# Optimization experiments

Measured on AMD Instinct MI355X. Metric: run time of the kernel, lower is better.

The kernel has to match this reference:

```python
import jax, jax.numpy as jnp
import numpy as np
import math

D_MODEL = 1024
N_HEADS = 16
HEAD_DIM = D_MODEL // N_HEADS
N_LEVELS = 4
B = 8
MAX_LEN = 1024
LN_EPS = 1e-5


def setup_inputs() -> dict:
    key = jax.random.key(0)
    ks = jax.random.split(key, 6)
    lengths = np.array([1024, 768, 512, 896, 640, 1024, 576, 704], dtype=np.int32)
    N = int(lengths.sum())  # 6144
    batch_offsets = jnp.asarray(np.concatenate([[0], np.cumsum(lengths)]).astype(np.int32))
    x = jax.random.normal(ks[0], (N, D_MODEL), jnp.float32)
    levels = jax.random.randint(ks[1], (N, 1), 0, N_LEVELS).astype(jnp.float32)
    coords = jax.random.uniform(ks[2], (N, 2), jnp.float32) * 64.0
    positions = jnp.concatenate([levels, coords], axis=-1)  # [N, 3] = (level, y, x)
    ln_gamma = jnp.ones((D_MODEL,), jnp.float32)
    ln_beta = jnp.zeros((D_MODEL,), jnp.float32)
    w_qkv = jax.random.normal(ks[3], (D_MODEL, 3 * D_MODEL), jnp.float32) / math.sqrt(D_MODEL)
    w_out = jax.random.normal(ks[4], (D_MODEL, D_MODEL), jnp.float32) / math.sqrt(D_MODEL)
    # learned per-level, per-head rotary frequencies for 2 spatial coords
    base = 10.0 ** (-2.0 * np.arange(HEAD_DIM // 2) / HEAD_DIM)  # rope_theta = 10.0
    rope_freqs = (jnp.asarray(base, jnp.float32)[None, None, :, None]
                  * (1.0 + 0.1 * jax.random.normal(ks[5], (N_LEVELS, N_HEADS, HEAD_DIM // 2, 2), jnp.float32)))
    return {"x": x, "positions": positions, "batch_offsets": batch_offsets,
            "ln_gamma": ln_gamma, "ln_beta": ln_beta, "w_qkv": w_qkv,
            "w_out": w_out, "rope_freqs": rope_freqs}


def _layernorm(x, g, b):
    mu = jnp.mean(x, axis=-1, keepdims=True)
    var = jnp.mean(jnp.square(x - mu), axis=-1, keepdims=True)
    return (x - mu) * jax.lax.rsqrt(var + LN_EPS) * g + b


def _forward(x, positions, batch_offsets, ln_gamma, ln_beta, w_qkv, w_out, rope_freqs):
    N = x.shape[0]
    residual = x
    h = _layernorm(x, ln_gamma, ln_beta)
    q, k, v = jnp.split(h @ w_qkv, 3, axis=-1)  # each [N, D]

    # ragged -> padded batch layout
    tok = jnp.arange(N)
    batch_ids = jnp.searchsorted(batch_offsets[1:], tok, side='right')  # [N]
    pos_in_seq = tok - batch_offsets[batch_ids]                         # [N]
    lengths = batch_offsets[1:] - batch_offsets[:-1]                    # [B]
    valid = jnp.arange(MAX_LEN)[None, :] < lengths[:, None]             # [B, L]

    def pad(t, fill=0.0):
        out = jnp.full((B, MAX_LEN) + t.shape[1:], fill, t.dtype)
        return out.at[batch_ids, pos_in_seq].set(t)

    qp = pad(q).reshape(B, MAX_LEN, N_HEADS, HEAD_DIM)
    kp = pad(k).reshape(B, MAX_LEN, N_HEADS, HEAD_DIM)
    vp = pad(v).reshape(B, MAX_LEN, N_HEADS, HEAD_DIM)
    posp = pad(positions, fill=1.0)  # padded positions filled with ones (as in torch code)

    # multilevel RoPE: per-level learned freqs over 2 spatial coords
    lvl = jnp.clip(posp[..., 0].astype(jnp.int32), 0, N_LEVELS - 1)  # [B, L]
    f = rope_freqs[lvl]                                              # [B, L, H, K, 2]
    ang = jnp.einsum('blhkc,blc->blhk', f, posp[..., 1:])            # [B, L, H, K]
    cos, sin = jnp.cos(ang), jnp.sin(ang)

    def rot(t):  # rotate consecutive pairs of head_dim
        t = t.reshape(B, MAX_LEN, N_HEADS, HEAD_DIM // 2, 2)
        a, b = t[..., 0], t[..., 1]
        return jnp.stack([a * cos - b * sin, a * sin + b * cos], axis=-1).reshape(
            B, MAX_LEN, N_HEADS, HEAD_DIM)

    qr, kr = rot(qp), rot(kp)

    # masked SDPA (padded keys excluded; padded query rows are dropped on un-pad)
    scale = 1.0 / math.sqrt(HEAD_DIM)
    scores = jnp.einsum('blhd,bmhd->bhlm', qr, kr) * scale
    scores = jnp.where(valid[:, None, None, :], scores, jnp.float32(-1e9))
    attn = jax.nn.softmax(scores, axis=-1)
    o = jnp.einsum('bhlm,bmhd->blhd', attn, vp).reshape(B, MAX_LEN, D_MODEL)

    o = o[batch_ids, pos_in_seq]  # back to packed [N, D]
    return o @ w_out + residual


def reference(x, positions, batch_offsets, ln_gamma, ln_beta, w_qkv, w_out, rope_freqs):
    return _forward(x, positions, batch_offsets, ln_gamma, ln_beta, w_qkv, w_out, rope_freqs)
```

## Files before the change

### kernel.cpp

```cpp
#include <hip/hip_runtime.h>


typedef float  f32x4  __attribute__((ext_vector_type(4)));
typedef __bf16 bf16x8 __attribute__((ext_vector_type(8)));
typedef __bf16 bf16x4 __attribute__((ext_vector_type(4)));
typedef short  s16x4  __attribute__((ext_vector_type(4)));
typedef short  s16x8  __attribute__((ext_vector_type(8)));
typedef unsigned short u16x4 __attribute__((ext_vector_type(4)));

typedef __attribute__((address_space(1))) void as1_void_t;
typedef __attribute__((address_space(3))) void as3_void_t;

static __device__ __forceinline__ unsigned short f2bf(float f) {
  unsigned int u = __float_as_uint(f);
  u += 0x7fffu + ((u >> 16) & 1u);
  return (unsigned short)(u >> 16);
}
static __device__ __forceinline__ float bf2f(unsigned short s) {
  return __uint_as_float(((unsigned int)s) << 16);
}

static __device__ __forceinline__ void gload_lds16(const void* g, void* l) {
  __builtin_amdgcn_global_load_lds((as1_void_t*)g, (as3_void_t*)l, 16, 0, 0);
}

static __device__ __forceinline__ f32x4 mfma32(bf16x8 a, bf16x8 b, f32x4 c) {
  return __builtin_amdgcn_mfma_f32_16x16x32_bf16(a, b, c, 0, 0, 0);
}
static __device__ __forceinline__ f32x4 mfma16(s16x4 a, s16x4 b, f32x4 c) {
  return __builtin_amdgcn_mfma_f32_16x16x16bf16_1k(a, b, c, 0, 0, 0);
}

__global__ __launch_bounds__(256) void ln_kernel(
    const float* __restrict__ x, const float* __restrict__ gamma,
    const float* __restrict__ beta, unsigned short* __restrict__ h, int Ntok) {
  int row  = blockIdx.x * 4 + (threadIdx.x >> 6);
  int lane = threadIdx.x & 63;
  const float* xr = x + (size_t)row * 1024;
  f32x4 v[4];
  float s = 0.f, ss = 0.f;
#pragma unroll
  for (int c = 0; c < 4; ++c) {
    v[c] = *(const f32x4*)(xr + c * 256 + lane * 4);
#pragma unroll
    for (int j = 0; j < 4; ++j) { s += v[c][j]; ss += v[c][j] * v[c][j]; }
  }
#pragma unroll
  for (int d = 1; d < 64; d <<= 1) {
    s  += __shfl_xor(s, d);
    ss += __shfl_xor(ss, d);
  }
  float mu  = s * (1.f / 1024.f);
  float var = ss * (1.f / 1024.f) - mu * mu;
  float inv = rsqrtf(var + 1e-5f);
#pragma unroll
  for (int c = 0; c < 4; ++c) {
    f32x4 gv = *(const f32x4*)(gamma + c * 256 + lane * 4);
    f32x4 bv = *(const f32x4*)(beta  + c * 256 + lane * 4);
    u16x4 hv;
#pragma unroll
    for (int j = 0; j < 4; ++j) hv[j] = f2bf((v[c][j] - mu) * inv * gv[j] + bv[j]);
    *(u16x4*)(h + (size_t)row * 1024 + c * 256 + lane * 4) = hv;
  }
}

__global__ __launch_bounds__(256) void transpose_bf16(
    const float* __restrict__ in, unsigned short* __restrict__ out, int R, int C) {
  __shared__ unsigned short tile[64][65];
  int c0 = blockIdx.x * 64, r0 = blockIdx.y * 64;
  int t = threadIdx.x;
  int tr = t >> 6, tc = t & 63;
#pragma unroll
  for (int i = 0; i < 16; ++i) {
    int rr = i * 4 + tr;
    tile[tc][rr] = f2bf(in[(size_t)(r0 + rr) * C + c0 + tc]);
  }
  __syncthreads();
#pragma unroll
  for (int i = 0; i < 16; ++i) {
    int cc = i * 4 + tr;
    out[(size_t)(c0 + cc) * R + r0 + tc] = tile[cc][tc];
  }
}

template <int MODE>
__global__ __launch_bounds__(256) void gemm_bt(
    const unsigned short* __restrict__ A, const unsigned short* __restrict__ Bt,
    const float* __restrict__ residual, float* __restrict__ Cf,
    unsigned short* __restrict__ Cqkv, int M, int Ncols, int K) {
  __shared__ unsigned short Alds[128 * 32];
  __shared__ unsigned short Blds[128 * 32];
  int n0 = blockIdx.x * 128, m0 = blockIdx.y * 128;
  int t = threadIdx.x, lane = t & 63, wave = t >> 6;
  int wr = wave >> 1, wc = wave & 1;
  int r = lane & 15, g = lane >> 4;
  f32x4 acc[4][4] = {};

  int srow = lane >> 2;
  int scol = (lane & 3) * 8;

  for (int k0 = 0; k0 < K; k0 += 32) {
    __syncthreads();
#pragma unroll
    for (int c = 0; c < 2; ++c) {
      int seg = wave * 2 + c;
      gload_lds16(A  + (size_t)(m0 + seg * 16 + srow) * K + k0 + scol,
                  Alds + seg * 16 * 32);
      gload_lds16(Bt + (size_t)(n0 + seg * 16 + srow) * K + k0 + scol,
                  Blds + seg * 16 * 32);
    }
    __syncthreads();
    bf16x8 a[4], b[4];
#pragma unroll
    for (int m = 0; m < 4; ++m)
      a[m] = *(const bf16x8*)(Alds + (wr * 64 + m * 16 + r) * 32 + g * 8);
#pragma unroll
    for (int n = 0; n < 4; ++n)
      b[n] = *(const bf16x8*)(Blds + (wc * 64 + n * 16 + r) * 32 + g * 8);
#pragma unroll
    for (int m = 0; m < 4; ++m)
#pragma unroll
      for (int n = 0; n < 4; ++n)
        acc[m][n] = mfma32(a[m], b[n], acc[m][n]);
  }

#pragma unroll
  for (int mi = 0; mi < 4; ++mi) {
    int grow0 = m0 + wr * 64 + mi * 16 + g * 4;
#pragma unroll
    for (int ni = 0; ni < 4; ++ni) {
      int gcol = n0 + wc * 64 + ni * 16 + r;
      f32x4 v = acc[mi][ni];
#pragma unroll
      for (int e = 0; e < 4; ++e) {
        int grow = grow0 + e;
        if (MODE == 0) {
          Cf[(size_t)grow * Ncols + gcol] =
              v[e] + residual[(size_t)grow * Ncols + gcol];
        } else {
          int which = gcol >> 10, rem = gcol & 1023, hh = rem >> 6, d = rem & 63;
          Cqkv[((size_t)(which * 16 + hh) * M + grow) * 64 + d] = f2bf(v[e]);
        }
      }
    }
  }
}

__global__ __launch_bounds__(256) void rope_kernel(
    unsigned short* __restrict__ QKV, const float* __restrict__ pos,
    const float* __restrict__ freqs, int Ntok) {
  int t = blockIdx.x * 256 + threadIdx.x;
  if (t >= Ntok * 512) return;
  int kk = t & 31, h = (t >> 5) & 15, i = t >> 9;
  float lvlf = pos[i * 3 + 0];
  float py   = pos[i * 3 + 1];
  float px   = pos[i * 3 + 2];
  int lvl = (int)lvlf;
  lvl = lvl < 0 ? 0 : (lvl > 3 ? 3 : lvl);
  const float* fp = freqs + (((lvl * 16 + h) * 32 + kk) << 1);
  float ang = fp[0] * py + fp[1] * px;
  float s, c;
  __sincosf(ang, &s, &c);
  size_t qoff = ((size_t)h * Ntok + i) * 64 + 2 * kk;
  size_t koff = qoff + (size_t)16 * Ntok * 64;
  unsigned int q2 = *(const unsigned int*)(QKV + qoff);
  float qa = bf2f((unsigned short)(q2 & 0xffff));
  float qb = bf2f((unsigned short)(q2 >> 16));
  *(unsigned int*)(QKV + qoff) =
      (unsigned int)f2bf(qa * c - qb * s) | ((unsigned int)f2bf(qa * s + qb * c) << 16);
  unsigned int k2 = *(const unsigned int*)(QKV + koff);
  float ka = bf2f((unsigned short)(k2 & 0xffff));
  float kb = bf2f((unsigned short)(k2 >> 16));
  *(unsigned int*)(QKV + koff) =
      (unsigned int)f2bf(ka * c - kb * s) | ((unsigned int)f2bf(ka * s + kb * c) << 16);
}

__global__ __launch_bounds__(128, 3) void attn_kernel(
    const unsigned short* __restrict__ QKV, const int* __restrict__ boff,
    unsigned short* __restrict__ O, int Ntok) {
  __shared__ unsigned short Klds[64][72];
  __shared__ unsigned short Vt[64][72];
  const float SCALE_LOG2 = 0.125f * 1.44269504088896340736f;

  int bid = blockIdx.x;
  int x = bid & 7, i = bid >> 3;
  int qblk = i & 15;
  int p = x + 8 * (i >> 4);
  int h = p & 15, b = p >> 4;
  int off = boff[b], len = boff[b + 1] - off;
  int q0 = qblk * 64;
  if (q0 >= len) return;
  int t = threadIdx.x, lane = t & 63, wave = t >> 6;
  int r = lane & 15, g = lane >> 4;
  const unsigned short* Qg = QKV + (size_t)h * Ntok * 64;
  const unsigned short* Kg = QKV + (size_t)(16 + h) * Ntok * 64;
  const unsigned short* Vg = QKV + (size_t)(32 + h) * Ntok * 64;
  int qmax = off + len - 1;

  bf16x8 qf[2][2];
#pragma unroll
  for (int qi = 0; qi < 2; ++qi) {
    int qtok = off + q0 + wave * 32 + qi * 16 + r;
    if (qtok > qmax) qtok = qmax;
#pragma unroll
    for (int c = 0; c < 2; ++c)
      qf[qi][c] = *(const bf16x8*)(Qg + (size_t)qtok * 64 + c * 32 + g * 8);
  }

  float m[2] = {-1e30f, -1e30f}, lsum[2] = {0.f, 0.f};
  f32x4 o[2][4] = {};

  int krow = t >> 1, kseg = t & 1;
  int vp = t & 31, vdc = t >> 5;

  s16x8 kr[4], va0, va1, vb0, vb1;
  {
    int ktok = off + krow; if (ktok > qmax) ktok = qmax;
#pragma unroll
    for (int c = 0; c < 4; ++c)
      kr[c] = *(const s16x8*)(Kg + (size_t)ktok * 64 + kseg * 32 + c * 8);
    int va = off + 2 * vp, vb = va + 1;
    if (va > qmax) va = qmax;
    if (vb > qmax) vb = qmax;
    va0 = *(const s16x8*)(Vg + (size_t)va * 64 + vdc * 16);
    va1 = *(const s16x8*)(Vg + (size_t)va * 64 + vdc * 16 + 8);
    vb0 = *(const s16x8*)(Vg + (size_t)vb * 64 + vdc * 16);
    vb1 = *(const s16x8*)(Vg + (size_t)vb * 64 + vdc * 16 + 8);
  }

  for (int kt = 0; kt < len; kt += 64) {
    __syncthreads();
#pragma unroll
    for (int c = 0; c < 4; ++c)
      *(s16x8*)&Klds[krow][kseg * 32 + c * 8] = kr[c];
#pragma unroll
    for (int j = 0; j < 8; ++j) {
      unsigned int p0 = (unsigned int)(unsigned short)va0[j] |
                        ((unsigned int)(unsigned short)vb0[j] << 16);
      unsigned int p1 = (unsigned int)(unsigned short)va1[j] |
                        ((unsigned int)(unsigned short)vb1[j] << 16);
      *(unsigned int*)&Vt[vdc * 16 + j][2 * vp]     = p0;
      *(unsigned int*)&Vt[vdc * 16 + 8 + j][2 * vp] = p1;
    }
    int ktn = kt + 64;
    if (ktn < len) {
      int ktok = off + ktn + krow; if (ktok > qmax) ktok = qmax;
#pragma unroll
      for (int c = 0; c < 4; ++c)
        kr[c] = *(const s16x8*)(Kg + (size_t)ktok * 64 + kseg * 32 + c * 8);
      int va = off + ktn + 2 * vp, vb = va + 1;
      if (va > qmax) va = qmax;
      if (vb > qmax) vb = qmax;
      va0 = *(const s16x8*)(Vg + (size_t)va * 64 + vdc * 16);
      va1 = *(const s16x8*)(Vg + (size_t)va * 64 + vdc * 16 + 8);
      vb0 = *(const s16x8*)(Vg + (size_t)vb * 64 + vdc * 16);
      vb1 = *(const s16x8*)(Vg + (size_t)vb * 64 + vdc * 16 + 8);
    }
    __syncthreads();

    f32x4 s[2][4];
    __builtin_amdgcn_s_setprio(1);
#pragma unroll
    for (int sub = 0; sub < 4; ++sub) {
      bf16x8 ka0 = *(const bf16x8*)(&Klds[sub * 16 + r][g * 8]);
      bf16x8 ka1 = *(const bf16x8*)(&Klds[sub * 16 + r][32 + g * 8]);
#pragma unroll
      for (int qi = 0; qi < 2; ++qi) {
        f32x4 acc = {};
        acc = mfma32(ka0, qf[qi][0], acc);
        acc = mfma32(ka1, qf[qi][1], acc);
        s[qi][sub] = acc;
      }
    }
    __builtin_amdgcn_s_setprio(0);

    bool tail = (kt + 64 > len);
    s16x4 pf[2][4];
#pragma unroll
    for (int qi = 0; qi < 2; ++qi) {
      float sc[4][4];
      float tmax = -1e30f;
#pragma unroll
      for (int sub = 0; sub < 4; ++sub)
#pragma unroll
        for (int e = 0; e < 4; ++e) {
          float v = s[qi][sub][e];
          if (tail && (kt + sub * 16 + 4 * g + e >= len)) v = -1e30f;
          sc[sub][e] = v;
          tmax = fmaxf(tmax, v);
        }
      float mq = m[qi];
      if (!__all(tmax * SCALE_LOG2 <= mq + 8.f)) {
        float tm = tmax * SCALE_LOG2;
        tm = fmaxf(tm, __shfl_xor(tm, 16));
        tm = fmaxf(tm, __shfl_xor(tm, 32));
        float mnew = fmaxf(mq, tm);
        float alpha = exp2f(mq - mnew);
        lsum[qi] *= alpha;
        m[qi] = mnew; mq = mnew;
        float al[4];
#pragma unroll
        for (int e = 0; e < 4; ++e) al[e] = __shfl(alpha, 4 * g + e);
#pragma unroll
        for (int dt = 0; dt < 4; ++dt)
#pragma unroll
          for (int e = 0; e < 4; ++e) o[qi][dt][e] *= al[e];
      }
      float psum = 0.f;
#pragma unroll
      for (int sub = 0; sub < 4; ++sub) {
        float pv[4];
        bf16x4 pb;
#pragma unroll
        for (int e = 0; e < 4; ++e) {
          pv[e] = exp2f(fmaf(sc[sub][e], SCALE_LOG2, -mq));
          psum += pv[e];
          pb[e] = (__bf16)pv[e];
        }
        pf[qi][sub] = __builtin_bit_cast(s16x4, pb);
      }
      psum += __shfl_xor(psum, 16);
      psum += __shfl_xor(psum, 32);
      lsum[qi] += psum;
    }

    __builtin_amdgcn_s_setprio(1);
#pragma unroll
    for (int dt = 0; dt < 4; ++dt)
#pragma unroll
      for (int sub = 0; sub < 4; ++sub) {
        s16x4 vf = *(const s16x4*)(&Vt[dt * 16 + r][sub * 16 + 4 * g]);
#pragma unroll
        for (int qi = 0; qi < 2; ++qi)
          o[qi][dt] = mfma16(pf[qi][sub], vf, o[qi][dt]);
      }
    __builtin_amdgcn_s_setprio(0);
  }

#pragma unroll
  for (int qi = 0; qi < 2; ++qi) {
    float inv = 1.0f / lsum[qi];
    float il[4];
#pragma unroll
    for (int e = 0; e < 4; ++e) il[e] = __shfl(inv, 4 * g + e);
#pragma unroll
    for (int dt = 0; dt < 4; ++dt)
#pragma unroll
      for (int e = 0; e < 4; ++e) {
        int tl = q0 + wave * 32 + qi * 16 + 4 * g + e;
        if (tl < len)
          O[(size_t)(off + tl) * 1024 + h * 64 + dt * 16 + r] =
              f2bf(o[qi][dt][e] * il[e]);
      }
  }
}

extern "C" void kernel_launch(void* const* d_in, const int* in_sizes, int n_in,
                              void* d_out, int out_size, void* d_ws, size_t ws_size,
                              hipStream_t stream) {
  const float* x     = (const float*)d_in[0];
  const float* pos   = (const float*)d_in[1];
  const int*   boff  = (const int*)d_in[2];
  const float* gamma = (const float*)d_in[3];
  const float* beta  = (const float*)d_in[4];
  const float* wqkv  = (const float*)d_in[5];
  const float* wout  = (const float*)d_in[6];
  const float* freqs = (const float*)d_in[7];
  float* out = (float*)d_out;
  int N  = in_sizes[0] / 1024;
  int Bn = in_sizes[2] - 1;

  char* ws = (char*)d_ws;
  unsigned short* wqkvT = (unsigned short*)ws;
  unsigned short* woutT = (unsigned short*)(ws + (size_t)3072 * 1024 * 2);
  unsigned short* QKV   = (unsigned short*)(ws + (size_t)3072 * 1024 * 2 +
                                            (size_t)1024 * 1024 * 2);
  size_t qkvBytes = (size_t)48 * N * 64 * 2;
  unsigned short* hbuf = (unsigned short*)((char*)QKV + qkvBytes);
  unsigned short* Obuf = hbuf;

  ln_kernel<<<N / 4, 256, 0, stream>>>(x, gamma, beta, hbuf, N);
  transpose_bf16<<<dim3(3072 / 64, 1024 / 64), 256, 0, stream>>>(wqkv, wqkvT, 1024, 3072);
  transpose_bf16<<<dim3(1024 / 64, 1024 / 64), 256, 0, stream>>>(wout, woutT, 1024, 1024);
  gemm_bt<1><<<dim3(3072 / 128, N / 128), 256, 0, stream>>>(
      hbuf, wqkvT, nullptr, nullptr, QKV, N, 3072, 1024);
  rope_kernel<<<(N * 512) / 256, 256, 0, stream>>>(QKV, pos, freqs, N);
  attn_kernel<<<Bn * 16 * 16, 128, 0, stream>>>(QKV, boff, Obuf, N);
  gemm_bt<0><<<dim3(1024 / 128, N / 128), 256, 0, stream>>>(
      Obuf, woutT, x, out, nullptr, N, 1024, 1024);
}
```

Before: 189.5 us.

## Fuse RoPE into QKV GEMM epilogue, store V transposed, compute softmax sums via MFMA

Rotary embedding moves into the QKV GEMM epilogue, using a lane shuffle to fetch each pair partner, so the separate rope kernel and its read-modify-write pass over Q and K go away. V is written transposed (head-dim major, token minor) so the attention kernel can copy it straight into LDS without the per-element pair packing. The softmax row sum is now an MFMA of P against a ones vector instead of shuffle reductions. Risks: the transposed V loads clamp reads near the sequence tail, and bf16-rounded P now feeds the denominator as well as the numerator.

```diff
diff --git a/kernel.cpp b/kernel.cpp
--- a/kernel.cpp
+++ b/kernel.cpp
@@ -87,7 +87,8 @@
 __global__ __launch_bounds__(256) void gemm_bt(
     const unsigned short* __restrict__ A, const unsigned short* __restrict__ Bt,
     const float* __restrict__ residual, float* __restrict__ Cf,
-    unsigned short* __restrict__ Cqkv, int M, int Ncols, int K) {
+    unsigned short* __restrict__ Cqkv, const float* __restrict__ pos,
+    const float* __restrict__ freqs, int M, int Ncols, int K) {
   __shared__ unsigned short Alds[128 * 32];
   __shared__ unsigned short Blds[128 * 32];
   int n0 = blockIdx.x * 128, m0 = blockIdx.y * 128;
@@ -124,55 +125,73 @@
         acc[m][n] = mfma32(a[m], b[n], acc[m][n]);
   }
 
-#pragma unroll
-  for (int mi = 0; mi < 4; ++mi) {
-    int grow0 = m0 + wr * 64 + mi * 16 + g * 4;
-#pragma unroll
-    for (int ni = 0; ni < 4; ++ni) {
-      int gcol = n0 + wc * 64 + ni * 16 + r;
-      f32x4 v = acc[mi][ni];
-#pragma unroll
-      for (int e = 0; e < 4; ++e) {
-        int grow = grow0 + e;
-        if (MODE == 0) {
-          Cf[(size_t)grow * Ncols + gcol] =
-              v[e] + residual[(size_t)grow * Ncols + gcol];
-        } else {
-          int which = gcol >> 10, rem = gcol & 1023, hh = rem >> 6, d = rem & 63;
-          Cqkv[((size_t)(which * 16 + hh) * M + grow) * 64 + d] = f2bf(v[e]);
+  if (MODE == 0) {
+#pragma unroll
+    for (int mi = 0; mi < 4; ++mi) {
+      int grow0 = m0 + wr * 64 + mi * 16 + g * 4;
+#pragma unroll
+      for (int ni = 0; ni < 4; ++ni) {
+        int gcol = n0 + wc * 64 + ni * 16 + r;
+        f32x4 v = acc[mi][ni];
+#pragma unroll
+        for (int e = 0; e < 4; ++e)
+          Cf[(size_t)(grow0 + e) * Ncols + gcol] =
+              v[e] + residual[(size_t)(grow0 + e) * Ncols + gcol];
+      }
+    }
+  } else {
+    int which = n0 >> 10;
+    if (which == 2) {
+      unsigned short* VtG = Cqkv + (size_t)32 * M * 64;
+#pragma unroll
+      for (int mi = 0; mi < 4; ++mi) {
+        int grow0 = m0 + wr * 64 + mi * 16 + g * 4;
+#pragma unroll
+        for (int ni = 0; ni < 4; ++ni) {
+          int gcol = n0 + wc * 64 + ni * 16 + r;
+          int rem = gcol & 1023, hh = rem >> 6, d = rem & 63;
+          f32x4 v = acc[mi][ni];
+          u16x4 hv;
+#pragma unroll
+          for (int e = 0; e < 4; ++e) hv[e] = f2bf(v[e]);
+          *(u16x4*)(VtG + (size_t)(hh * 64 + d) * M + grow0) = hv;
         }
       }
-    }
-  }
-}
-
-__global__ __launch_bounds__(256) void rope_kernel(
-    unsigned short* __restrict__ QKV, const float* __restrict__ pos,
-    const float* __restrict__ freqs, int Ntok) {
-  int t = blockIdx.x * 256 + threadIdx.x;
-  if (t >= Ntok * 512) return;
-  int kk = t & 31, h = (t >> 5) & 15, i = t >> 9;
-  float lvlf = pos[i * 3 + 0];
-  float py   = pos[i * 3 + 1];
-  float px   = pos[i * 3 + 2];
-  int lvl = (int)lvlf;
-  lvl = lvl < 0 ? 0 : (lvl > 3 ? 3 : lvl);
-  const float* fp = freqs + (((lvl * 16 + h) * 32 + kk) << 1);
-  float ang = fp[0] * py + fp[1] * px;
-  float s, c;
-  __sincosf(ang, &s, &c);
-  size_t qoff = ((size_t)h * Ntok + i) * 64 + 2 * kk;
-  size_t koff = qoff + (size_t)16 * Ntok * 64;
-  unsigned int q2 = *(const unsigned int*)(QKV + qoff);
-  float qa = bf2f((unsigned short)(q2 & 0xffff));
-  float qb = bf2f((unsigned short)(q2 >> 16));
-  *(unsigned int*)(QKV + qoff) =
-      (unsigned int)f2bf(qa * c - qb * s) | ((unsigned int)f2bf(qa * s + qb * c) << 16);
-  unsigned int k2 = *(const unsigned int*)(QKV + koff);
-  float ka = bf2f((unsigned short)(k2 & 0xffff));
-  float kb = bf2f((unsigned short)(k2 >> 16));
-  *(unsigned int*)(QKV + koff) =
-      (unsigned int)f2bf(ka * c - kb * s) | ((unsigned int)f2bf(ka * s + kb * c) << 16);
+    } else {
+#pragma unroll
+      for (int mi = 0; mi < 4; ++mi) {
+        int grow0 = m0 + wr * 64 + mi * 16 + g * 4;
+        float py[4], px[4];
+        int lv[4];
+#pragma unroll
+        for (int e = 0; e < 4; ++e) {
+          int tk = grow0 + e;
+          int l = (int)pos[tk * 3 + 0];
+          lv[e] = l < 0 ? 0 : (l > 3 ? 3 : l);
+          py[e] = pos[tk * 3 + 1];
+          px[e] = pos[tk * 3 + 2];
+        }
+#pragma unroll
+        for (int ni = 0; ni < 4; ++ni) {
+          int gcol = n0 + wc * 64 + ni * 16 + r;
+          int rem = gcol & 1023, hh = rem >> 6, d = rem & 63;
+          int kk = d >> 1, par = d & 1;
+          f32x4 v = acc[mi][ni];
+#pragma unroll
+          for (int e = 0; e < 4; ++e) {
+            float other = __shfl_xor(v[e], 1);
+            const float* fp = freqs + (((lv[e] * 16 + hh) * 32 + kk) << 1);
+            float ang = fp[0] * py[e] + fp[1] * px[e];
+            float sn, cs;
+            __sincosf(ang, &sn, &cs);
+            float vc = v[e] * cs;
+            float res = par ? fmaf(other, sn, vc) : fmaf(other, -sn, vc);
+            Cqkv[((size_t)(which * 16 + hh) * M + grow0 + e) * 64 + d] = f2bf(res);
+          }
+        }
+      }
+    }
+  }
 }
 
 __global__ __launch_bounds__(128, 3) void attn_kernel(
@@ -181,6 +200,7 @@
   __shared__ unsigned short Klds[64][72];
   __shared__ unsigned short Vt[64][72];
   const float SCALE_LOG2 = 0.125f * 1.44269504088896340736f;
+  const s16x4 ones16 = {(short)0x3F80, (short)0x3F80, (short)0x3F80, (short)0x3F80};
 
   int bid = blockIdx.x;
   int x = bid & 7, i = bid >> 3;
@@ -194,7 +214,7 @@
   int r = lane & 15, g = lane >> 4;
   const unsigned short* Qg = QKV + (size_t)h * Ntok * 64;
   const unsigned short* Kg = QKV + (size_t)(16 + h) * Ntok * 64;
-  const unsigned short* Vg = QKV + (size_t)(32 + h) * Ntok * 64;
+  const unsigned short* VtG = QKV + (size_t)32 * Ntok * 64;
   int qmax = off + len - 1;
 
   bf16x8 qf[2][2];
@@ -207,54 +227,46 @@
       qf[qi][c] = *(const bf16x8*)(Qg + (size_t)qtok * 64 + c * 32 + g * 8);
   }
 
-  float m[2] = {-1e30f, -1e30f}, lsum[2] = {0.f, 0.f};
+  float m[2] = {-1e30f, -1e30f};
   f32x4 o[2][4] = {};
-
-  int krow = t >> 1, kseg = t & 1;
-  int vp = t & 31, vdc = t >> 5;
-
-  s16x8 kr[4], va0, va1, vb0, vb1;
+  f32x4 o_sum[2] = {};
+
+  int srow = t >> 1, sseg = t & 1;
+  const unsigned short* Vrow = VtG + (size_t)(h * 64 + srow) * Ntok;
+
+  s16x8 kr[4], vr[4];
   {
-    int ktok = off + krow; if (ktok > qmax) ktok = qmax;
+    int ktok = off + srow; if (ktok > qmax) ktok = qmax;
 #pragma unroll
     for (int c = 0; c < 4; ++c)
-      kr[c] = *(const s16x8*)(Kg + (size_t)ktok * 64 + kseg * 32 + c * 8);
-    int va = off + 2 * vp, vb = va + 1;
-    if (va > qmax) va = qmax;
-    if (vb > qmax) vb = qmax;
-    va0 = *(const s16x8*)(Vg + (size_t)va * 64 + vdc * 16);
-    va1 = *(const s16x8*)(Vg + (size_t)va * 64 + vdc * 16 + 8);
-    vb0 = *(const s16x8*)(Vg + (size_t)vb * 64 + vdc * 16);
-    vb1 = *(const s16x8*)(Vg + (size_t)vb * 64 + vdc * 16 + 8);
+      kr[c] = *(const s16x8*)(Kg + (size_t)ktok * 64 + sseg * 32 + c * 8);
+    int ts = sseg * 32;
+    if (ts + 8 > len) ts = len - 8;
+#pragma unroll
+    for (int c = 0; c < 4; ++c) {
+      int tc = ts + c * 8; if (tc + 8 > len) tc = len - 8;
+      vr[c] = *(const s16x8*)(Vrow + off + tc);
+    }
   }
 
   for (int kt = 0; kt < len; kt += 64) {
     __syncthreads();
 #pragma unroll
-    for (int c = 0; c < 4; ++c)
-      *(s16x8*)&Klds[krow][kseg * 32 + c * 8] = kr[c];
-#pragma unroll
-    for (int j = 0; j < 8; ++j) {
-      unsigned int p0 = (unsigned int)(unsigned short)va0[j] |
-                        ((unsigned int)(unsigned short)vb0[j] << 16);
-      unsigned int p1 = (unsigned int)(unsigned short)va1[j] |
-                        ((unsigned int)(unsigned short)vb1[j] << 16);
-      *(unsigned int*)&Vt[vdc * 16 + j][2 * vp]     = p0;
-      *(unsigned int*)&Vt[vdc * 16 + 8 + j][2 * vp] = p1;
+    for (int c = 0; c < 4; ++c) {
+      *(s16x8*)&Klds[srow][sseg * 32 + c * 8] = kr[c];
+      *(s16x8*)&Vt[srow][sseg * 32 + c * 8]   = vr[c];
     }
     int ktn = kt + 64;
     if (ktn < len) {
-      int ktok = off + ktn + krow; if (ktok > qmax) ktok = qmax;
+      int ktok = off + ktn + srow; if (ktok > qmax) ktok = qmax;
 #pragma unroll
       for (int c = 0; c < 4; ++c)
-        kr[c] = *(const s16x8*)(Kg + (size_t)ktok * 64 + kseg * 32 + c * 8);
-      int va = off + ktn + 2 * vp, vb = va + 1;
-      if (va > qmax) va = qmax;
-      if (vb > qmax) vb = qmax;
-      va0 = *(const s16x8*)(Vg + (size_t)va * 64 + vdc * 16);
-      va1 = *(const s16x8*)(Vg + (size_t)va * 64 + vdc * 16 + 8);
-      vb0 = *(const s16x8*)(Vg + (size_t)vb * 64 + vdc * 16);
-      vb1 = *(const s16x8*)(Vg + (size_t)vb * 64 + vdc * 16 + 8);
+        kr[c] = *(const s16x8*)(Kg + (size_t)ktok * 64 + sseg * 32 + c * 8);
+#pragma unroll
+      for (int c = 0; c < 4; ++c) {
+        int tc = ktn + sseg * 32 + c * 8; if (tc + 8 > len) tc = len - 8;
+        vr[c] = *(const s16x8*)(Vrow + off + tc);
+      }
     }
     __syncthreads();
 
@@ -279,16 +291,19 @@
 #pragma unroll
     for (int qi = 0; qi < 2; ++qi) {
       float sc[4][4];
-      float tmax = -1e30f;
-#pragma unroll
-      for (int sub = 0; sub < 4; ++sub)
+      float ms[4];
+#pragma unroll
+      for (int sub = 0; sub < 4; ++sub) {
 #pragma unroll
         for (int e = 0; e < 4; ++e) {
           float v = s[qi][sub][e];
           if (tail && (kt + sub * 16 + 4 * g + e >= len)) v = -1e30f;
           sc[sub][e] = v;
-          tmax = fmaxf(tmax, v);
         }
+        ms[sub] = fmaxf(fmaxf(sc[sub][0], sc[sub][1]),
+                        fmaxf(sc[sub][2], sc[sub][3]));
+      }
+      float tmax = fmaxf(fmaxf(ms[0], ms[1]), fmaxf(ms[2], ms[3]));
       float mq = m[qi];
       if (!__all(tmax * SCALE_LOG2 <= mq + 8.f)) {
         float tm = tmax * SCALE_LOG2;
@@ -296,35 +311,30 @@
         tm = fmaxf(tm, __shfl_xor(tm, 32));
         float mnew = fmaxf(mq, tm);
         float alpha = exp2f(mq - mnew);
-        lsum[qi] *= alpha;
         m[qi] = mnew; mq = mnew;
-        float al[4];
-#pragma unroll
-        for (int e = 0; e < 4; ++e) al[e] = __shfl(alpha, 4 * g + e);
+#pragma unroll
+        for (int e = 0; e < 4; ++e) o_sum[qi][e] *= alpha;
 #pragma unroll
         for (int dt = 0; dt < 4; ++dt)
 #pragma unroll
-          for (int e = 0; e < 4; ++e) o[qi][dt][e] *= al[e];
-      }
-      float psum = 0.f;
+          for (int e = 0; e < 4; ++e) o[qi][dt][e] *= alpha;
+      }
 #pragma unroll
       for (int sub = 0; sub < 4; ++sub) {
-        float pv[4];
         bf16x4 pb;
 #pragma unroll
-        for (int e = 0; e < 4; ++e) {
-          pv[e] = exp2f(fmaf(sc[sub][e], SCALE_LOG2, -mq));
-          psum += pv[e];
-          pb[e] = (__bf16)pv[e];
-        }
+        for (int e = 0; e < 4; ++e)
+          pb[e] = (__bf16)exp2f(fmaf(sc[sub][e], SCALE_LOG2, -mq));
         pf[qi][sub] = __builtin_bit_cast(s16x4, pb);
       }
-      psum += __shfl_xor(psum, 16);
-      psum += __shfl_xor(psum, 32);
-      lsum[qi] += psum;
     }
 
     __builtin_amdgcn_s_setprio(1);
+#pragma unroll
+    for (int sub = 0; sub < 4; ++sub) {
+      o_sum[0] = mfma16(pf[0][sub], ones16, o_sum[0]);
+      o_sum[1] = mfma16(pf[1][sub], ones16, o_sum[1]);
+    }
 #pragma unroll
     for (int dt = 0; dt < 4; ++dt)
 #pragma unroll
@@ -339,10 +349,9 @@
 
 #pragma unroll
   for (int qi = 0; qi < 2; ++qi) {
-    float inv = 1.0f / lsum[qi];
     float il[4];
 #pragma unroll
-    for (int e = 0; e < 4; ++e) il[e] = __shfl(inv, 4 * g + e);
+    for (int e = 0; e < 4; ++e) il[e] = 1.0f / o_sum[qi][e];
 #pragma unroll
     for (int dt = 0; dt < 4; ++dt)
 #pragma unroll
@@ -383,9 +392,8 @@
   transpose_bf16<<<dim3(3072 / 64, 1024 / 64), 256, 0, stream>>>(wqkv, wqkvT, 1024, 3072);
   transpose_bf16<<<dim3(1024 / 64, 1024 / 64), 256, 0, stream>>>(wout, woutT, 1024, 1024);
   gemm_bt<1><<<dim3(3072 / 128, N / 128), 256, 0, stream>>>(
-      hbuf, wqkvT, nullptr, nullptr, QKV, N, 3072, 1024);
-  rope_kernel<<<(N * 512) / 256, 256, 0, stream>>>(QKV, pos, freqs, N);
+      hbuf, wqkvT, nullptr, nullptr, QKV, pos, freqs, N, 3072, 1024);
   attn_kernel<<<Bn * 16 * 16, 128, 0, stream>>>(QKV, boff, Obuf, N);
   gemm_bt<0><<<dim3(1024 / 128, N / 128), 256, 0, stream>>>(
-      Obuf, woutT, x, out, nullptr, N, 1024, 1024);
-}
+      Obuf, woutT, x, out, nullptr, nullptr, nullptr, N, 1024, 1024);
+}
```

After: 200.1 us. 5.6% more time.

## Pre-transpose V in a separate kernel and compute softmax row sums via MFMA

Applied to the files above, without the earlier changes.

A new kernel transposes V into a head-major, dimension-by-token global buffer. The attention kernel can then stage V tiles into LDS with plain vector copies instead of interleaving token pairs per element. The softmax denominator is now accumulated by an MFMA against a vector of bf16 ones, which drops the per-tile shuffle reductions and the alpha broadcast shuffles. This costs an extra launch plus a full read and write of V, and the output buffer now reuses the original V region.

```diff
diff --git a/kernel.cpp b/kernel.cpp
--- a/kernel.cpp
+++ b/kernel.cpp
@@ -175,12 +175,42 @@
       (unsigned int)f2bf(ka * c - kb * s) | ((unsigned int)f2bf(ka * s + kb * c) << 16);
 }
 
+__global__ __launch_bounds__(256) void vtrans_kernel(
+    const unsigned short* __restrict__ Vp, unsigned short* __restrict__ VtG,
+    int Ntok) {
+  __shared__ unsigned short tile[64][72];
+  int blk = blockIdx.x;
+  int h = blk & 15, t0 = (blk >> 4) * 64;
+  int t = threadIdx.x;
+  {
+    int tok = t >> 2, dc = (t & 3) * 16;
+    const unsigned short* src = Vp + ((size_t)h * Ntok + t0 + tok) * 64 + dc;
+    *(s16x8*)&tile[tok][dc]     = *(const s16x8*)src;
+    *(s16x8*)&tile[tok][dc + 8] = *(const s16x8*)(src + 8);
+  }
+  __syncthreads();
+  {
+    int d = t >> 2, tc = (t & 3) * 16;
+    s16x8 o0, o1;
+#pragma unroll
+    for (int j = 0; j < 8; ++j) {
+      o0[j] = (short)tile[tc + j][d];
+      o1[j] = (short)tile[tc + 8 + j][d];
+    }
+    unsigned short* dst = VtG + (size_t)(h * 64 + d) * Ntok + t0 + tc;
+    *(s16x8*)dst       = o0;
+    *(s16x8*)(dst + 8) = o1;
+  }
+}
+
 __global__ __launch_bounds__(128, 3) void attn_kernel(
-    const unsigned short* __restrict__ QKV, const int* __restrict__ boff,
+    const unsigned short* __restrict__ QKV,
+    const unsigned short* __restrict__ VtG, const int* __restrict__ boff,
     unsigned short* __restrict__ O, int Ntok) {
   __shared__ unsigned short Klds[64][72];
   __shared__ unsigned short Vt[64][72];
   const float SCALE_LOG2 = 0.125f * 1.44269504088896340736f;
+  const s16x4 ones16 = {(short)0x3F80, (short)0x3F80, (short)0x3F80, (short)0x3F80};
 
   int bid = blockIdx.x;
   int x = bid & 7, i = bid >> 3;
@@ -194,7 +224,6 @@
   int r = lane & 15, g = lane >> 4;
   const unsigned short* Qg = QKV + (size_t)h * Ntok * 64;
   const unsigned short* Kg = QKV + (size_t)(16 + h) * Ntok * 64;
-  const unsigned short* Vg = QKV + (size_t)(32 + h) * Ntok * 64;
   int qmax = off + len - 1;
 
   bf16x8 qf[2][2];
@@ -207,54 +236,44 @@
       qf[qi][c] = *(const bf16x8*)(Qg + (size_t)qtok * 64 + c * 32 + g * 8);
   }
 
-  float m[2] = {-1e30f, -1e30f}, lsum[2] = {0.f, 0.f};
+  float m[2] = {-1e30f, -1e30f};
   f32x4 o[2][4] = {};
-
-  int krow = t >> 1, kseg = t & 1;
-  int vp = t & 31, vdc = t >> 5;
-
-  s16x8 kr[4], va0, va1, vb0, vb1;
+  f32x4 o_sum[2] = {};
+
+  int srow = t >> 1, sseg = t & 1;
+  const unsigned short* Vrow = VtG + (size_t)(h * 64 + srow) * Ntok;
+
+  s16x8 kr[4], vr[4];
   {
-    int ktok = off + krow; if (ktok > qmax) ktok = qmax;
+    int ktok = off + srow; if (ktok > qmax) ktok = qmax;
 #pragma unroll
     for (int c = 0; c < 4; ++c)
-      kr[c] = *(const s16x8*)(Kg + (size_t)ktok * 64 + kseg * 32 + c * 8);
-    int va = off + 2 * vp, vb = va + 1;
-    if (va > qmax) va = qmax;
-    if (vb > qmax) vb = qmax;
-    va0 = *(const s16x8*)(Vg + (size_t)va * 64 + vdc * 16);
-    va1 = *(const s16x8*)(Vg + (size_t)va * 64 + vdc * 16 + 8);
-    vb0 = *(const s16x8*)(Vg + (size_t)vb * 64 + vdc * 16);
-    vb1 = *(const s16x8*)(Vg + (size_t)vb * 64 + vdc * 16 + 8);
+      kr[c] = *(const s16x8*)(Kg + (size_t)ktok * 64 + sseg * 32 + c * 8);
+#pragma unroll
+    for (int c = 0; c < 4; ++c) {
+      int tc = sseg * 32 + c * 8; if (tc + 8 > len) tc = len - 8;
+      vr[c] = *(const s16x8*)(Vrow + off + tc);
+    }
   }
 
   for (int kt = 0; kt < len; kt += 64) {
     __syncthreads();
 #pragma unroll
-    for (int c = 0; c < 4; ++c)
-      *(s16x8*)&Klds[krow][kseg * 32 + c * 8] = kr[c];
-#pragma unroll
-    for (int j = 0; j < 8; ++j) {
-      unsigned int p0 = (unsigned int)(unsigned short)va0[j] |
-                        ((unsigned int)(unsigned short)vb0[j] << 16);
-      unsigned int p1 = (unsigned int)(unsigned short)va1[j] |
-                        ((unsigned int)(unsigned short)vb1[j] << 16);
-      *(unsigned int*)&Vt[vdc * 16 + j][2 * vp]     = p0;
-      *(unsigned int*)&Vt[vdc * 16 + 8 + j][2 * vp] = p1;
+    for (int c = 0; c < 4; ++c) {
+      *(s16x8*)&Klds[srow][sseg * 32 + c * 8] = kr[c];
+      *(s16x8*)&Vt[srow][sseg * 32 + c * 8]   = vr[c];
     }
     int ktn = kt + 64;
     if (ktn < len) {
-      int ktok = off + ktn + krow; if (ktok > qmax) ktok = qmax;
+      int ktok = off + ktn + srow; if (ktok > qmax) ktok = qmax;
 #pragma unroll
       for (int c = 0; c < 4; ++c)
-        kr[c] = *(const s16x8*)(Kg + (size_t)ktok * 64 + kseg * 32 + c * 8);
-      int va = off + ktn + 2 * vp, vb = va + 1;
-      if (va > qmax) va = qmax;
-      if (vb > qmax) vb = qmax;
-      va0 = *(const s16x8*)(Vg + (size_t)va * 64 + vdc * 16);
-      va1 = *(const s16x8*)(Vg + (size_t)va * 64 + vdc * 16 + 8);
-      vb0 = *(const s16x8*)(Vg + (size_t)vb * 64 + vdc * 16);
-      vb1 = *(const s16x8*)(Vg + (size_t)vb * 64 + vdc * 16 + 8);
+        kr[c] = *(const s16x8*)(Kg + (size_t)ktok * 64 + sseg * 32 + c * 8);
+#pragma unroll
+      for (int c = 0; c < 4; ++c) {
+        int tc = ktn + sseg * 32 + c * 8; if (tc + 8 > len) tc = len - 8;
+        vr[c] = *(const s16x8*)(Vrow + off + tc);
+      }
     }
     __syncthreads();
 
@@ -279,16 +298,19 @@
 #pragma unroll
     for (int qi = 0; qi < 2; ++qi) {
       float sc[4][4];
-      float tmax = -1e30f;
-#pragma unroll
-      for (int sub = 0; sub < 4; ++sub)
+      float ms[4];
+#pragma unroll
+      for (int sub = 0; sub < 4; ++sub) {
 #pragma unroll
         for (int e = 0; e < 4; ++e) {
           float v = s[qi][sub][e];
           if (tail && (kt + sub * 16 + 4 * g + e >= len)) v = -1e30f;
           sc[sub][e] = v;
-          tmax = fmaxf(tmax, v);
         }
+        ms[sub] = fmaxf(fmaxf(sc[sub][0], sc[sub][1]),
+                        fmaxf(sc[sub][2], sc[sub][3]));
+      }
+      float tmax = fmaxf(fmaxf(ms[0], ms[1]), fmaxf(ms[2], ms[3]));
       float mq = m[qi];
       if (!__all(tmax * SCALE_LOG2 <= mq + 8.f)) {
         float tm = tmax * SCALE_LOG2;
@@ -296,35 +318,30 @@
         tm = fmaxf(tm, __shfl_xor(tm, 32));
         float mnew = fmaxf(mq, tm);
         float alpha = exp2f(mq - mnew);
-        lsum[qi] *= alpha;
         m[qi] = mnew; mq = mnew;
-        float al[4];
-#pragma unroll
-        for (int e = 0; e < 4; ++e) al[e] = __shfl(alpha, 4 * g + e);
+#pragma unroll
+        for (int e = 0; e < 4; ++e) o_sum[qi][e] *= alpha;
 #pragma unroll
         for (int dt = 0; dt < 4; ++dt)
 #pragma unroll
-          for (int e = 0; e < 4; ++e) o[qi][dt][e] *= al[e];
-      }
-      float psum = 0.f;
+          for (int e = 0; e < 4; ++e) o[qi][dt][e] *= alpha;
+      }
 #pragma unroll
       for (int sub = 0; sub < 4; ++sub) {
-        float pv[4];
         bf16x4 pb;
 #pragma unroll
-        for (int e = 0; e < 4; ++e) {
-          pv[e] = exp2f(fmaf(sc[sub][e], SCALE_LOG2, -mq));
-          psum += pv[e];
-          pb[e] = (__bf16)pv[e];
-        }
+        for (int e = 0; e < 4; ++e)
+          pb[e] = (__bf16)exp2f(fmaf(sc[sub][e], SCALE_LOG2, -mq));
         pf[qi][sub] = __builtin_bit_cast(s16x4, pb);
       }
-      psum += __shfl_xor(psum, 16);
-      psum += __shfl_xor(psum, 32);
-      lsum[qi] += psum;
     }
 
     __builtin_amdgcn_s_setprio(1);
+#pragma unroll
+    for (int sub = 0; sub < 4; ++sub) {
+      o_sum[0] = mfma16(pf[0][sub], ones16, o_sum[0]);
+      o_sum[1] = mfma16(pf[1][sub], ones16, o_sum[1]);
+    }
 #pragma unroll
     for (int dt = 0; dt < 4; ++dt)
 #pragma unroll
@@ -339,10 +356,9 @@
 
 #pragma unroll
   for (int qi = 0; qi < 2; ++qi) {
-    float inv = 1.0f / lsum[qi];
     float il[4];
 #pragma unroll
-    for (int e = 0; e < 4; ++e) il[e] = __shfl(inv, 4 * g + e);
+    for (int e = 0; e < 4; ++e) il[e] = 1.0f / o_sum[qi][e];
 #pragma unroll
     for (int dt = 0; dt < 4; ++dt)
 #pragma unroll
@@ -377,7 +393,9 @@
                                             (size_t)1024 * 1024 * 2);
   size_t qkvBytes = (size_t)48 * N * 64 * 2;
   unsigned short* hbuf = (unsigned short*)((char*)QKV + qkvBytes);
-  unsigned short* Obuf = hbuf;
+  unsigned short* VtG  = hbuf;
+  unsigned short* Vp   = QKV + (size_t)32 * N * 64;
+  unsigned short* Obuf = Vp;
 
   ln_kernel<<<N / 4, 256, 0, stream>>>(x, gamma, beta, hbuf, N);
   transpose_bf16<<<dim3(3072 / 64, 1024 / 64), 256, 0, stream>>>(wqkv, wqkvT, 1024, 3072);
@@ -385,7 +403,8 @@
   gemm_bt<1><<<dim3(3072 / 128, N / 128), 256, 0, stream>>>(
       hbuf, wqkvT, nullptr, nullptr, QKV, N, 3072, 1024);
   rope_kernel<<<(N * 512) / 256, 256, 0, stream>>>(QKV, pos, freqs, N);
-  attn_kernel<<<Bn * 16 * 16, 128, 0, stream>>>(QKV, boff, Obuf, N);
+  vtrans_kernel<<<16 * (N / 64), 256, 0, stream>>>(Vp, VtG, N);
+  attn_kernel<<<Bn * 16 * 16, 128, 0, stream>>>(QKV, VtG, boff, Obuf, N);
   gemm_bt<0><<<dim3(1024 / 128, N / 128), 256, 0, stream>>>(
       Obuf, woutT, x, out, nullptr, N, 1024, 1024);
 }
```

Result: no change. 191.3 us (+1.0%).
